# Performance work log

Measured on AMD Instinct MI355X. Metric: run time of the kernel, lower is better.

The kernel has to match this reference:

```python
import jax, jax.numpy as jnp
import numpy as np

B, T, D = 16, 2048, 128   # batch, seq_len, input_size
H, L = 256, 2             # hidden_size, rnn layers
N1, N2 = 32, 32           # head output sizes


def _rnn_dir(x, Wih, Whh, bih, bhh, reverse):
    # x: [B, T, din] -> outputs [B, T, H]; torch RNN tanh cell:
    # h_t = tanh(W_ih x_t + b_ih + W_hh h_{t-1} + b_hh), h_0 = 0
    xT = jnp.swapaxes(x, 0, 1)            # [T, B, din]
    if reverse:
        xT = xT[::-1]
    pre = xT @ Wih.T + (bih + bhh)        # batch input projection once
    h0 = jnp.zeros((x.shape[0], Whh.shape[0]), x.dtype)
    def step(h, u):
        h = jnp.tanh(u + h @ Whh.T)
        return h, h
    _, hs = jax.lax.scan(step, h0, pre)   # [T, B, H]
    if reverse:
        hs = hs[::-1]
    return jnp.swapaxes(hs, 0, 1)         # [B, T, H]


def _birnn(x, params):
    out = x
    for l in range(L):
        Wf, Uf, bf, cf, Wb, Ub, bb, cb = params[l]
        fwd = _rnn_dir(out, Wf, Uf, bf, cf, reverse=False)
        bwd = _rnn_dir(out, Wb, Ub, bb, cb, reverse=True)
        out = jnp.concatenate([fwd, bwd], axis=-1)  # [B, T, 2H]
    return out


def _head(h, W1, b1, W2, b2):
    # fc1 -> relu -> fc2, fully batched over [B, T]
    z = jax.nn.relu(jnp.einsum('bth,kh->btk', h, W1) + b1)
    return jnp.einsum('btk,nk->btn', z, W2) + b2


def setup_inputs() -> dict:
    key = jax.random.key(0)
    ks = iter(jax.random.split(key, 40))
    def p(shape):
        return jax.random.normal(next(ks), shape, jnp.float32) * 0.05
    inp = {"x": jax.random.normal(next(ks), (B, T, D), jnp.float32)}
    for l in range(L):
        din = D if l == 0 else 2 * H
        for d in ("f", "b"):
            inp[f"Wih{l}{d}"] = p((H, din))
            inp[f"Whh{l}{d}"] = p((H, H))
            inp[f"bih{l}{d}"] = p((H,))
            inp[f"bhh{l}{d}"] = p((H,))
    for t, n in (("t1", N1), ("t2", N2)):
        inp[f"W1{t}"] = p((H // 2, 2 * H))
        inp[f"b1{t}"] = p((H // 2,))
        inp[f"W2{t}"] = p((n, H // 2))
        inp[f"b2{t}"] = p((n,))
    return inp


def reference(x,
              Wih0f, Whh0f, bih0f, bhh0f, Wih0b, Whh0b, bih0b, bhh0b,
              Wih1f, Whh1f, bih1f, bhh1f, Wih1b, Whh1b, bih1b, bhh1b,
              W1t1, b1t1, W2t1, b2t1, W1t2, b1t2, W2t2, b2t2):
    params = [
        (Wih0f, Whh0f, bih0f, bhh0f, Wih0b, Whh0b, bih0b, bhh0b),
        (Wih1f, Whh1f, bih1f, bhh1f, Wih1b, Whh1b, bih1b, bhh1b),
    ]
    out = _birnn(x, params)                       # [B, T, 2H]
    y1 = _head(out, W1t1, b1t1, W2t1, b2t1)       # [B, T, N1]
    y2 = _head(out, W1t2, b1t2, W2t2, b2t2)       # [B, T, N2]
    return (y1, y2)
```

## Files before the change

kernel.cpp:

```cpp
#include <hip/hip_runtime.h>
#include <hip/hip_fp16.h>

typedef _Float16 half2_t __attribute__((ext_vector_type(2)));
typedef _Float16 half8_t __attribute__((ext_vector_type(8)));
typedef float f32x4 __attribute__((ext_vector_type(4)));

struct __align__(16) H2x4 { half2_t h[4]; };
struct __align__(8)  H2x2 { half2_t h[2]; };

__device__ __forceinline__ float fdot2f(half2_t a, half2_t b, float c){
#if __has_builtin(__builtin_amdgcn_fdot2)
  return __builtin_amdgcn_fdot2(a, b, c, false);
#else
  return c + (float)a[0]*(float)b[0] + (float)a[1]*(float)b[1];
#endif
}

__device__ __forceinline__ float fast_exp2f(float x){
#if __has_builtin(__builtin_amdgcn_exp2f)
  return __builtin_amdgcn_exp2f(x);
#else
  return __expf(x*0.6931471805599453f);
#endif
}

__device__ __forceinline__ void pin8(half8_t &x){ asm volatile("" : "+v"(x)); }

struct PrepArgs {
  const float* src[13];
  __half* dst[13];
  int n[13];
};
__global__ __launch_bounds__(256) void prep_cast_k(PrepArgs a){
  const int r = blockIdx.y;
  const int n = a.n[r];
  const float* __restrict__ s = a.src[r];
  __half* __restrict__ d = a.dst[r];
  for (int i = blockIdx.x*256 + threadIdx.x; i < n; i += gridDim.x*256)
    d[i] = __float2half(s[i]);
}

struct BiasArgs {
  const float *bih0f,*bhh0f,*bih0b,*bhh0b,*bih1f,*bhh1f,*bih1b,*bhh1b;
  const float *b1t1,*b1t2,*b2t1,*b2t2;
  float *b0,*b1,*bz,*by;
};
__global__ __launch_bounds__(256) void prep_bias_k(BiasArgs a){
  const int i = threadIdx.x;
  if (i < 256){
    a.b0[i]     = a.bih0f[i] + a.bhh0f[i];
    a.b0[256+i] = a.bih0b[i] + a.bhh0b[i];
    a.b1[i]     = a.bih1f[i] + a.bhh1f[i];
    a.b1[256+i] = a.bih1b[i] + a.bhh1b[i];
  }
  if (i < 128){ a.bz[i] = a.b1t1[i]; a.bz[128+i] = a.b1t2[i]; }
  if (i < 32){  a.by[i] = a.b2t1[i]; a.by[32+i]  = a.b2t2[i]; }
}

template<int AMODE, int MODE>
__global__ __launch_bounds__(256,2) void gemm_nt_k(
    const __half* __restrict__ A, const __half* __restrict__ B,
    __half* __restrict__ C, const float* __restrict__ bias,
    int M, int N, int K)
{
  __shared__ __align__(16) _Float16 As[128*40];
  __shared__ __align__(16) _Float16 Bs[128*40];
  const int tid = threadIdx.x;
  const int wave = tid>>6, lane = tid&63;
  const int wr = wave>>1, wc = wave&1;
  const int lrow = lane&15, lk = lane>>4;
  const int m0 = blockIdx.x*128, n0 = blockIdx.y*128;
  f32x4 acc[4][4];
  #pragma unroll
  for (int i=0;i<4;i++)
    #pragma unroll
    for (int j=0;j<4;j++) acc[i][j] = (f32x4){0.f,0.f,0.f,0.f};

  for (int k0=0; k0<K; k0+=32){
    __syncthreads();
    #pragma unroll
    for (int i=0;i<2;i++){
      int idx = i*256 + tid;
      int row = idx>>2, ch = idx&3;
      const __half* ap;
      if (AMODE==0){
        ap = A + (size_t)(m0+row)*K + k0 + ch*8;
      } else {
        const int m = m0+row, b = m>>11, tt = m&2047;
        const int k = k0 + ch*8, dirr = k>>8, rr = k&255;
        ap = A + ((size_t)(dirr*2048 + tt)*16 + b)*256 + rr;
      }
      const int4 av = *(const int4*)ap;
      const int4 bv = *(const int4*)(B + (size_t)(n0+row)*K + k0 + ch*8);
      *(int4*)(As + row*40 + ch*8) = av;
      *(int4*)(Bs + row*40 + ch*8) = bv;
    }
    __syncthreads();
    half8_t af[4], bf[4];
    #pragma unroll
    for (int mi=0;mi<4;mi++) af[mi] = *(const half8_t*)(As + (wr*64+mi*16+lrow)*40 + lk*8);
    #pragma unroll
    for (int ni=0;ni<4;ni++) bf[ni] = *(const half8_t*)(Bs + (wc*64+ni*16+lrow)*40 + lk*8);
    #pragma unroll
    for (int mi=0;mi<4;mi++)
      #pragma unroll
      for (int ni=0;ni<4;ni++)
        acc[mi][ni] = __builtin_amdgcn_mfma_f32_16x16x32_f16(af[mi], bf[ni], acc[mi][ni], 0,0,0);
  }
  #pragma unroll
  for (int mi=0;mi<4;mi++){
    #pragma unroll
    for (int ni=0;ni<4;ni++){
      const int n = n0 + wc*64 + ni*16 + lrow;
      const float bv = bias[n];
      #pragma unroll
      for (int r2=0;r2<4;r2++){
        const int m = m0 + wr*64 + mi*16 + lk*4 + r2;
        float v = acc[mi][ni][r2] + bv;
        if (MODE==1){
          C[(size_t)m*256 + n] = __float2half(fmaxf(v, 0.f));
        } else {
          const int dir = n>>8, row = n&255;
          const int b = m>>11, t = m&2047;
          const size_t di = (((size_t)(dir*2048 + t)*64 + (row>>2))*16 + (size_t)b)*4 + (row&3);
          C[di] = __float2half(v);
        }
      }
    }
  }
}

__device__ __forceinline__ void rnn_step(
    const half8_t (&af)[4][8], uint2 (&P)[4],
    const uint2*& pp, long pstep, bool do_prefetch,
    const _Float16* cur, _Float16* nxt,
    __half*& op, long ostep,
    int wave, int lb, int lk)
{
  f32x4 a0[4], a1[4];
  #pragma unroll
  for (int mt=0;mt<4;++mt){
    H2x2 q = __builtin_bit_cast(H2x2, P[mt]);
    a0[mt] = (f32x4){(float)q.h[0][0], (float)q.h[0][1], (float)q.h[1][0], (float)q.h[1][1]};
    a1[mt] = (f32x4){0.f,0.f,0.f,0.f};
  }
  if (do_prefetch){
    #pragma unroll
    for (int mt=0;mt<4;++mt) P[mt] = pp[mt*64];
    pp += pstep;
  }
  half8_t bf[8];
  #pragma unroll
  for (int kt=0;kt<8;++kt){
    const int row = kt*4 + lk;
    bf[kt] = *(const half8_t*)(cur + row*128 + ((lb+row)&15)*8);
  }
  #pragma unroll
  for (int kt=0;kt<4;++kt){
    #pragma unroll
    for (int mt=0;mt<4;++mt){
      a0[mt] = __builtin_amdgcn_mfma_f32_16x16x32_f16(af[mt][kt],   bf[kt],   a0[mt], 0,0,0);
      a1[mt] = __builtin_amdgcn_mfma_f32_16x16x32_f16(af[mt][kt+4], bf[kt+4], a1[mt], 0,0,0);
    }
  }
  #pragma unroll
  for (int mt=0;mt<4;++mt){
    float h[4];
    #pragma unroll
    for (int i=0;i<4;++i){
      const float u  = a0[mt][i] + a1[mt][i];
      const float e2 = fast_exp2f(u * 2.8853900817779268f);
      h[i] = fmaf(-2.f, __builtin_amdgcn_rcpf(1.f + e2), 1.f);
    }
    half2_t hlo; hlo[0]=(_Float16)h[0]; hlo[1]=(_Float16)h[1];
    half2_t hhi; hhi[0]=(_Float16)h[2]; hhi[1]=(_Float16)h[3];
    H2x2 pk2; pk2.h[0]=hlo; pk2.h[1]=hhi;
    const uint2 pv = __builtin_bit_cast(uint2, pk2);
    *(uint2*)(op + mt*16) = pv;
    const int rw = wave*8 + mt*2 + (lk>>1);
    *(uint2*)(nxt + rw*128 + ((lb+rw)&15)*8 + (lk&1)*4) = pv;
  }
  op += ostep;
  asm volatile("s_waitcnt lgkmcnt(0)" ::: "memory");
  __builtin_amdgcn_s_barrier();
  __builtin_amdgcn_sched_barrier(0);
}

__global__ __launch_bounds__(256,1) void rnn_mfma_k(
    const __half* __restrict__ preM, const __half* __restrict__ whh,
    __half* __restrict__ hblk, int T)
{
  const int dir  = blockIdx.x;
  const int tid  = threadIdx.x;
  const int wave = tid>>6, lane = tid&63;
  const int lb = lane&15;
  const int lk = lane>>4;

  half8_t af[4][8];
  {
    const __half* wp = whh + (size_t)dir*65536;
    #pragma unroll
    for (int mt=0;mt<4;++mt)
      #pragma unroll
      for (int kt=0;kt<8;++kt)
        af[mt][kt] = *(const half8_t*)(wp + (size_t)(wave*64 + mt*16 + lb)*256 + kt*32 + lk*8);
  }
  #pragma unroll
  for (int mt=0;mt<4;++mt)
    #pragma unroll
    for (int kt=0;kt<8;++kt) pin8(af[mt][kt]);

  __shared__ __align__(16) _Float16 hbuf[2][4096];
  {
    uint4 z = {0u,0u,0u,0u};
    *(uint4*)(&hbuf[0][tid*16])     = z;
    *(uint4*)(&hbuf[0][tid*16 + 8]) = z;
  }

  const uint2* preu2 = (const uint2*)preM;
  const int poff = (wave*16 + lk)*16 + lb;
  const long pstep = dir ? -1024L : 1024L;
  uint2 pA[4], pB[4];
  {
    const int tt0 = dir ? (T-1) : 0;
    const uint2* ps = preu2 + (size_t)(dir*T + tt0)*1024 + poff;
    #pragma unroll
    for (int mt=0;mt<4;++mt) pA[mt] = ps[mt*64];
  }
  {
    const int tt1 = dir ? (T-2) : 1;
    const uint2* ps = preu2 + (size_t)(dir*T + tt1)*1024 + poff;
    #pragma unroll
    for (int mt=0;mt<4;++mt) pB[mt] = ps[mt*64];
  }
  const uint2* pp = preu2 + (size_t)(dir*T + (dir ? T-3 : 2))*1024 + poff;

  const int tt0 = dir ? (T-1) : 0;
  __half* op = hblk + ((size_t)(dir*2048 + tt0)*16 + lb)*256 + wave*64 + lk*4;
  const long ostep = dir ? -4096L : 4096L;

  __syncthreads();

  for (int t=0; t<T; t+=2){
    rnn_step(af, pA, pp, pstep, t+2<T, &hbuf[0][0], &hbuf[1][0], op, ostep, wave, lb, lk);
    rnn_step(af, pB, pp, pstep, t+3<T, &hbuf[1][0], &hbuf[0][0], op, ostep, wave, lb, lk);
  }
}

__global__ __launch_bounds__(256,4) void head2_k(
    const __half* __restrict__ z, const __half* __restrict__ w2,
    const float* __restrict__ by, float* __restrict__ yout)
{
  __shared__ _Float16 w2s[64*130];
  __shared__ __align__(16) _Float16 zs[4*256];
  const int tid = threadIdx.x;
  {
    const half2_t* g = (const half2_t*)w2;
    for (int idx=tid; idx<4096; idx+=256){
      int row=idx>>6, c=idx&63;
      *(half2_t*)(w2s + row*130 + c*2) = g[idx];
    }
  }
  const int m0 = blockIdx.x*4;
  if (tid < 128){
    const int4* g = (const int4*)(z + (size_t)m0*256);
    *(int4*)(zs + (tid>>5)*256 + (tid&31)*8) = g[tid];
  }
  __syncthreads();
  const int r = tid>>6, n = tid&63;
  const int head = n>>5;
  const half2_t* zp = (const half2_t*)(zs + r*256) + head*64;
  const half2_t* wp = (const half2_t*)(w2s + n*130);
  float acc0=by[n], acc1=0.f;
  #pragma unroll
  for (int j=0;j<64;j+=2){
    acc0 = fdot2f(zp[j],   wp[j],   acc0);
    acc1 = fdot2f(zp[j+1], wp[j+1], acc1);
  }
  yout[(size_t)head*1048576 + (size_t)(m0+r)*32 + (n&31)] = acc0+acc1;
}

extern "C" void kernel_launch(void* const* d_in, const int* in_sizes, int n_in,
                              void* d_out, int out_size, void* d_ws, size_t ws_size,
                              hipStream_t stream)
{
  (void)in_sizes; (void)n_in; (void)out_size; (void)ws_size;
  const float* X    =(const float*)d_in[0];
  const float* Wih0f=(const float*)d_in[1];
  const float* Whh0f=(const float*)d_in[2];
  const float* bih0f=(const float*)d_in[3];
  const float* bhh0f=(const float*)d_in[4];
  const float* Wih0b=(const float*)d_in[5];
  const float* Whh0b=(const float*)d_in[6];
  const float* bih0b=(const float*)d_in[7];
  const float* bhh0b=(const float*)d_in[8];
  const float* Wih1f=(const float*)d_in[9];
  const float* Whh1f=(const float*)d_in[10];
  const float* bih1f=(const float*)d_in[11];
  const float* bhh1f=(const float*)d_in[12];
  const float* Wih1b=(const float*)d_in[13];
  const float* Whh1b=(const float*)d_in[14];
  const float* bih1b=(const float*)d_in[15];
  const float* bhh1b=(const float*)d_in[16];
  const float* W1t1 =(const float*)d_in[17];
  const float* b1t1 =(const float*)d_in[18];
  const float* W2t1 =(const float*)d_in[19];
  const float* b2t1 =(const float*)d_in[20];
  const float* W1t2 =(const float*)d_in[21];
  const float* b1t2 =(const float*)d_in[22];
  const float* W2t2 =(const float*)d_in[23];
  const float* b2t2 =(const float*)d_in[24];

  char* ws = (char*)d_ws;
  size_t off = 0;
  auto alloc = [&](size_t bytes)->void*{ void* p = ws + off; off += (bytes + 1023) & ~(size_t)1023; return p; };
  __half* x16  = (__half*)alloc((size_t)4194304*2);
  __half* wih0 = (__half*)alloc((size_t)65536*2);
  __half* whh0 = (__half*)alloc((size_t)131072*2);
  __half* wih1 = (__half*)alloc((size_t)262144*2);
  __half* whh1 = (__half*)alloc((size_t)131072*2);
  __half* w1   = (__half*)alloc((size_t)131072*2);
  __half* w2   = (__half*)alloc((size_t)8192*2);
  float* b0 = (float*)alloc(512*4);
  float* b1 = (float*)alloc(512*4);
  float* bz = (float*)alloc(256*4);
  float* by = (float*)alloc(64*4);
  __half* preM  = (__half*)alloc((size_t)16777216*2);
  __half* hblk0 = (__half*)alloc((size_t)16777216*2);
  __half* hblk1 = (__half*)alloc((size_t)16777216*2);

  PrepArgs pa;
  auto set=[&](int r, const float* s, __half* d, int n){ pa.src[r]=s; pa.dst[r]=d; pa.n[r]=n; };
  set(0, X, x16, 4194304);
  set(1, Wih0f, wih0, 32768);       set(2, Wih0b, wih0+32768, 32768);
  set(3, Whh0f, whh0, 65536);       set(4, Whh0b, whh0+65536, 65536);
  set(5, Wih1f, wih1, 131072);      set(6, Wih1b, wih1+131072, 131072);
  set(7, Whh1f, whh1, 65536);       set(8, Whh1b, whh1+65536, 65536);
  set(9, W1t1, w1, 65536);          set(10, W1t2, w1+65536, 65536);
  set(11, W2t1, w2, 4096);          set(12, W2t2, w2+4096, 4096);
  prep_cast_k<<<dim3(1024,13),256,0,stream>>>(pa);

  BiasArgs ba = {bih0f,bhh0f,bih0b,bhh0b,bih1f,bhh1f,bih1b,bhh1b,b1t1,b1t2,b2t1,b2t2,b0,b1,bz,by};
  prep_bias_k<<<1,256,0,stream>>>(ba);

  gemm_nt_k<0,0><<<dim3(256,4),256,0,stream>>>(x16, wih0, preM, b0, 32768,512,128);
  rnn_mfma_k<<<2,256,0,stream>>>(preM, whh0, hblk0, 2048);
  gemm_nt_k<1,0><<<dim3(256,4),256,0,stream>>>(hblk0, wih1, preM, b1, 32768,512,512);
  rnn_mfma_k<<<2,256,0,stream>>>(preM, whh1, hblk1, 2048);
  gemm_nt_k<1,1><<<dim3(256,2),256,0,stream>>>(hblk1, w1, preM, bz, 32768,256,512);
  head2_k<<<8192,256,0,stream>>>(preM, w2, by, (float*)d_out);
}
```

Before: 3.325 ms.

## Keep recurrent weights in AGPRs, use inline-asm MFMA, drop LDS swizzle

The recurrent weight fragments are pinned to accumulation registers (AGPRs) and fed to hand-written MFMA instructions that read A from AGPRs, freeing VGPRs in the serial RNN step. Manual s_nop fences cover MFMA hazards around the inline asm. The XOR-style swizzle on hidden-state LDS reads and writes is removed, and fp16 packing switches to cvt_pkrtz (round-toward-zero). This risks more LDS bank conflicts, hand-placed hazard padding that may be too short or wasteful, and a small precision change from truncating rounding.

```diff
diff --git a/kernel.cpp b/kernel.cpp
--- a/kernel.cpp
+++ b/kernel.cpp
@@ -24,7 +24,27 @@
 #endif
 }
 
-__device__ __forceinline__ void pin8(half8_t &x){ asm volatile("" : "+v"(x)); }
+__device__ __forceinline__ half2_t pkrtz(float lo, float hi){
+  return __builtin_bit_cast(half2_t, __builtin_amdgcn_cvt_pkrtz(lo, hi));
+}
+
+__device__ __forceinline__ void pinA(half8_t &x){ asm volatile("" : "+a"(x)); }
+
+__device__ __forceinline__ void mfma_av(f32x4 &c, const half8_t &a, const half8_t &b){
+  asm("v_mfma_f32_16x16x32_f16 %0, %1, %2, %0"
+      : "+v"(c) : "a"(a), "v"(b));
+}
+
+__device__ __forceinline__ void accfence_pre(f32x4 (&a0)[4], f32x4 (&a1)[4]){
+  asm volatile("s_nop 1"
+    : "+v"(a0[0]),"+v"(a0[1]),"+v"(a0[2]),"+v"(a0[3]),
+      "+v"(a1[0]),"+v"(a1[1]),"+v"(a1[2]),"+v"(a1[3]));
+}
+__device__ __forceinline__ void accfence_post(f32x4 (&a0)[4], f32x4 (&a1)[4]){
+  asm volatile("s_nop 7\n\ts_nop 7"
+    : "+v"(a0[0]),"+v"(a0[1]),"+v"(a0[2]),"+v"(a0[3]),
+      "+v"(a1[0]),"+v"(a1[1]),"+v"(a1[2]),"+v"(a1[3]));
+}
 
 struct PrepArgs {
   const float* src[13];
@@ -151,18 +171,18 @@
   }
   half8_t bf[8];
   #pragma unroll
-  for (int kt=0;kt<8;++kt){
-    const int row = kt*4 + lk;
-    bf[kt] = *(const half8_t*)(cur + row*128 + ((lb+row)&15)*8);
-  }
+  for (int kt=0;kt<8;++kt)
+    bf[kt] = *(const half8_t*)(cur + (kt*4 + lk)*128 + lb*8);
+  accfence_pre(a0, a1);
   #pragma unroll
   for (int kt=0;kt<4;++kt){
     #pragma unroll
     for (int mt=0;mt<4;++mt){
-      a0[mt] = __builtin_amdgcn_mfma_f32_16x16x32_f16(af[mt][kt],   bf[kt],   a0[mt], 0,0,0);
-      a1[mt] = __builtin_amdgcn_mfma_f32_16x16x32_f16(af[mt][kt+4], bf[kt+4], a1[mt], 0,0,0);
-    }
-  }
+      mfma_av(a0[mt], af[mt][kt],   bf[kt]);
+      mfma_av(a1[mt], af[mt][kt+4], bf[kt+4]);
+    }
+  }
+  accfence_post(a0, a1);
   #pragma unroll
   for (int mt=0;mt<4;++mt){
     float h[4];
@@ -172,13 +192,13 @@
       const float e2 = fast_exp2f(u * 2.8853900817779268f);
       h[i] = fmaf(-2.f, __builtin_amdgcn_rcpf(1.f + e2), 1.f);
     }
-    half2_t hlo; hlo[0]=(_Float16)h[0]; hlo[1]=(_Float16)h[1];
-    half2_t hhi; hhi[0]=(_Float16)h[2]; hhi[1]=(_Float16)h[3];
-    H2x2 pk2; pk2.h[0]=hlo; pk2.h[1]=hhi;
+    H2x2 pk2;
+    pk2.h[0] = pkrtz(h[0], h[1]);
+    pk2.h[1] = pkrtz(h[2], h[3]);
     const uint2 pv = __builtin_bit_cast(uint2, pk2);
     *(uint2*)(op + mt*16) = pv;
     const int rw = wave*8 + mt*2 + (lk>>1);
-    *(uint2*)(nxt + rw*128 + ((lb+rw)&15)*8 + (lk&1)*4) = pv;
+    *(uint2*)(nxt + rw*128 + lb*8 + (lk&1)*4) = pv;
   }
   op += ostep;
   asm volatile("s_waitcnt lgkmcnt(0)" ::: "memory");
@@ -208,7 +228,7 @@
   #pragma unroll
   for (int mt=0;mt<4;++mt)
     #pragma unroll
-    for (int kt=0;kt<8;++kt) pin8(af[mt][kt]);
+    for (int kt=0;kt<8;++kt) pinA(af[mt][kt]);
 
   __shared__ __align__(16) _Float16 hbuf[2][4096];
   {
```

Measured after the change: 3.415 ms. 2.7% more time.
